# Performance work log

Measured on AMD Instinct MI355X. Metric: run time of the kernel, lower is better.

## Reference

```python
import jax, jax.numpy as jnp
import numpy as np

C_IN = 12      # total channels (rgb-noised + hidden)
C_NOISE = 3    # noise-prediction channels
HID = 128      # rule-MLP hidden size
PERC = 48      # perception channels (depthwise, 48/12 = 4 filters per channel)
TDIM = 256     # sinusoidal time-embedding dim


def setup_inputs() -> dict:
    key = jax.random.key(0)
    ks = jax.random.split(key, 12)
    B, H, W = 16, 256, 256
    x = jax.random.normal(ks[0], (B, C_NOISE, H, W), jnp.float32)
    hidden_channels = jax.random.normal(ks[1], (B, C_IN - C_NOISE, H, W), jnp.float32)
    t = jax.random.randint(ks[2], (B,), 0, 1000)
    # depthwise 3x3 perceive conv: torch weight shape [out=48, in/groups=1, 3, 3]
    w_perceive = jax.random.normal(ks[3], (PERC, 1, 3, 3), jnp.float32) * 0.1
    b_perceive = jax.random.normal(ks[4], (PERC,), jnp.float32) * 0.01
    # 1x1 convs of the rule network, stored as [out, in]
    w1 = jax.random.normal(ks[5], (HID, PERC), jnp.float32) * 0.1
    b1 = jax.random.normal(ks[6], (HID,), jnp.float32) * 0.01
    w2 = jax.random.normal(ks[7], (HID, HID), jnp.float32) * 0.05
    b2 = jax.random.normal(ks[8], (HID,), jnp.float32) * 0.01
    # conv3 is zero-initialized in the original; random here for test coverage
    w3 = jax.random.normal(ks[9], (C_IN, HID), jnp.float32) * 0.05
    # time embedding Linear(256 -> c_noise)
    w_time = jax.random.normal(ks[10], (C_NOISE, TDIM), jnp.float32) * 0.1
    b_time = jax.random.normal(ks[11], (C_NOISE,), jnp.float32) * 0.01
    return dict(x=x, hidden_channels=hidden_channels, t=t,
                w_perceive=w_perceive, b_perceive=b_perceive,
                w1=w1, b1=b1, w2=w2, b2=b2, w3=w3,
                w_time=w_time, b_time=b_time)


def _pos_encoding(t, channels):
    # t: [B] int -> [B, channels] sinusoidal embedding (torch repeat-then-scale layout)
    inv_freq = 1.0 / (10000.0 ** (jnp.arange(0, channels, 2, dtype=jnp.float32) / channels))
    ang = t.astype(jnp.float32)[:, None] * inv_freq  # [B, channels//2]
    return jnp.concatenate([jnp.sin(ang), jnp.cos(ang)], axis=-1)


def reference(x, hidden_channels, t, w_perceive, b_perceive, w1, b1, w2, b2, w3, w_time, b_time):
    # concat noised channels with hidden state channels -> [B, 12, H, W]
    xf = jnp.concatenate([x, hidden_channels], axis=1)
    # depthwise 3x3 conv, 'same' padding, groups = C_IN
    perc = jax.lax.conv_general_dilated(
        xf, w_perceive, window_strides=(1, 1), padding='SAME',
        feature_group_count=C_IN,
        dimension_numbers=('NCHW', 'OIHW', 'NCHW')) + b_perceive[None, :, None, None]
    # rule network: three 1x1 convs (pointwise MLP) with ReLUs
    h = jax.nn.relu(jnp.einsum('bchw,oc->bohw', perc, w1) + b1[None, :, None, None])
    h = jax.nn.relu(jnp.einsum('bchw,oc->bohw', h, w2) + b2[None, :, None, None])
    out = jnp.einsum('bchw,oc->bohw', h, w3)  # no bias
    # time embedding: sinusoidal -> SiLU -> Linear -> broadcast over H, W
    pe = _pos_encoding(t, TDIM)                       # [B, 256]
    emb = jax.nn.silu(pe) @ w_time.T + b_time         # [B, 3]
    noise_prediction = out[:, :C_NOISE] + emb[:, :, None, None]
    hidden_out = out[:, C_NOISE:]
    return (hidden_out, noise_prediction)
```

## Files before the change

### kernel.cpp

```cpp
#include <hip/hip_runtime.h>


#define ACT_S 136
#define NOISE_BASE 9437184

#define WSF_OFF 17408
#define WSF_B1 0
#define WSF_B2 128
#define WSF_EMB 256

typedef short bf16x8 __attribute__((ext_vector_type(8)));
typedef float f32x4 __attribute__((ext_vector_type(4)));

__device__ __forceinline__ short f2bf(float f) {
    union { float f; unsigned u; } cv; cv.f = f;
    unsigned r = cv.u + 0x7FFFu + ((cv.u >> 16) & 1u);
    return (short)(r >> 16);
}
__device__ __forceinline__ unsigned pk2bf(float f0, float f1) {
    union { float f; unsigned u; } a, b; a.f = f0; b.f = f1;
    return __builtin_amdgcn_perm(b.u + 0x8000u, a.u + 0x8000u, 0x07060302u);
}

__device__ __forceinline__ int permch(int f) {
    return (f & ~31) + 8 * ((f & 15) >> 2) + 4 * ((f >> 4) & 1) + (f & 3);
}

__global__ void prep_emb_kernel(const float* __restrict__ wpg, const float* __restrict__ bpg,
                                const float* __restrict__ w1g, const float* __restrict__ b1g,
                                const float* __restrict__ w2g, const float* __restrict__ b2g,
                                const float* __restrict__ w3g,
                                const int* __restrict__ t,
                                const float* __restrict__ wt, const float* __restrict__ bt,
                                short* __restrict__ wsb, float* __restrict__ wsf)
{
    const int bid = blockIdx.x, tid = threadIdx.x;
    if (bid < 64) {
        int i = bid * 256 + tid;
        int f = i >> 7, kk = i & 127;
        int o = permch(f);
        int qq = kk >> 5, r = kk & 31;
        float v = 0.f;
        if (r < 30 && (r % 10) < 9) {
            int c3 = r / 10, k = r % 10;
            int ic = 3 * qq + c3;
            #pragma unroll
            for (int j = 0; j < 4; ++j)
                v += w1g[o * 48 + 4 * ic + j] * wpg[(4 * ic + j) * 9 + k];
        }
        wsb[i] = f2bf(v);
        return;
    }
    if (bid < 128) {
        int i = (bid - 64) * 256 + tid;
        int f = i >> 7, col = i & 127;
        wsb[16384 + i] = f2bf(w2g[permch(f) * 128 + col]);
        return;
    }
    if (bid == 128) {
        for (int j = tid; j < 2048; j += 256)
            wsb[32768 + j] = (j < 1536) ? f2bf(w3g[j]) : (short)0;
        return;
    }
    if (bid == 129) {
        if (tid < 128) {
            float s = b1g[tid];
            #pragma unroll 4
            for (int c = 0; c < 48; ++c) s += w1g[tid * 48 + c] * bpg[c];
            wsf[WSF_B1 + tid] = s;
        } else {
            wsf[WSF_B2 + (tid - 128)] = b2g[tid - 128];
        }
        return;
    }
    int b = bid - 130;
    int lane = threadIdx.x;
    if (lane >= 64) return;
    float tv = (float)t[b];
    float s0 = 0.f, s1 = 0.f, s2 = 0.f;
    const float LOG1E4 = 9.210340371976184f;
    #pragma unroll
    for (int ii = 0; ii < 2; ++ii) {
        int i = lane + ii * 64;
        float invf = __expf(-LOG1E4 * (float)i * (1.0f / 128.0f));
        float ang = tv * invf;
        float sn = sinf(ang), cs = cosf(ang);
        float ss = sn / (1.0f + __expf(-sn));
        float sc = cs / (1.0f + __expf(-cs));
        s0 += ss * wt[0 * 256 + i] + sc * wt[0 * 256 + i + 128];
        s1 += ss * wt[1 * 256 + i] + sc * wt[1 * 256 + i + 128];
        s2 += ss * wt[2 * 256 + i] + sc * wt[2 * 256 + i + 128];
    }
    #pragma unroll
    for (int off = 32; off; off >>= 1) {
        s0 += __shfl_down(s0, off);
        s1 += __shfl_down(s1, off);
        s2 += __shfl_down(s2, off);
    }
    if (lane == 0) {
        wsf[WSF_EMB + b * 3 + 0] = s0 + bt[0];
        wsf[WSF_EMB + b * 3 + 1] = s1 + bt[1];
        wsf[WSF_EMB + b * 3 + 2] = s2 + bt[2];
    }
}

__global__ __launch_bounds__(256, 3) void canet_main(
    const float* __restrict__ xg,
    const float* __restrict__ hg,
    const short* __restrict__ wsb,
    const float* __restrict__ wsf,
    float* __restrict__ outg)
{
    __shared__ __align__(16) short bufA[64 * ACT_S];
    __shared__ __align__(16) short h1S[64 * ACT_S];
    __shared__ __align__(16) short w3_s[16 * 128];
    __shared__ __align__(16) float bias_s[256];

    const int tid = threadIdx.x;
    const int b = blockIdx.x >> 8;
    const int y = blockIdx.x & 255;

    bias_s[tid] = wsf[WSF_B1 + tid];
    for (int i = tid; i < 2048; i += 256) {
        int row = i >> 7, col = i & 127;
        w3_s[(row << 7) + (col ^ ((row & 7) << 3))] = wsb[32768 + i];
    }

    const int wv = tid >> 6;
    const int lane = tid & 63;
    const int m = lane & 15;
    const int q = lane >> 4;

    bf16x8 w1f[2][4], w2f[2][4];
    #pragma unroll
    for (int j = 0; j < 2; ++j) {
        int n = wv * 32 + j * 16 + m;
        #pragma unroll
        for (int ks = 0; ks < 4; ++ks) {
            w1f[j][ks] = *(const bf16x8*)(wsb + n * 128 + ks * 32 + q * 8);
            w2f[j][ks] = *(const bf16x8*)(wsb + 16384 + n * 128 + ks * 32 + q * 8);
        }
    }
    const float embv = (m < 3) ? wsf[WSF_EMB + b * 3 + m] : 0.0f;

    const float* src3[3];
    #pragma unroll
    for (int i3 = 0; i3 < 3; ++i3) {
        int ic = 3 * q + i3;
        src3[i3] = (ic < 3) ? (xg + (((size_t)b * 3 + ic) << 16))
                            : (hg + (((size_t)b * 9 + (ic - 3)) << 16));
    }
    int yoff[3]; bool yokk[3];
    #pragma unroll
    for (int ky = 0; ky < 3; ++ky) {
        int yy = y + ky - 1;
        yokk[ky] = (yy >= 0) && (yy < 256);
        yoff[ky] = (yokk[ky] ? yy : y) * 256;
    }

    auto load_taps = [&](float (&tp)[27], int pxl) {
        const int xm1 = pxl - (pxl > 0);
        const int xp1 = pxl + (pxl < 255);
        #pragma unroll
        for (int i3 = 0; i3 < 3; ++i3) {
            #pragma unroll
            for (int ky = 0; ky < 3; ++ky) {
                const float* rp = src3[i3] + yoff[ky];
                tp[i3 * 9 + ky * 3 + 0] = rp[xm1];
                tp[i3 * 9 + ky * 3 + 1] = rp[pxl];
                tp[i3 * 9 + ky * 3 + 2] = rp[xp1];
            }
        }
    };

    const int w3sw = (m & 7) << 3;

    float tp[27];
    load_taps(tp, wv * 16 + m);

    __syncthreads();

    for (int it = 0; it < 4; ++it) {
        const int x0 = it * 64;
        const int px = x0 + wv * 16 + m;

        {
            const bool okl = (px > 0), okr = (px < 255);
            short* prow = bufA + (wv * 16 + m) * ACT_S + 32 * q;
            unsigned rr[16];
            rr[15] = 0u;
            #pragma unroll
            for (int i3 = 0; i3 < 3; ++i3) {
                float tm[9];
                #pragma unroll
                for (int ky = 0; ky < 3; ++ky) {
                    int o = i3 * 9 + ky * 3;
                    tm[ky * 3 + 0] = (yokk[ky] && okl) ? tp[o + 0] : 0.0f;
                    tm[ky * 3 + 1] = yokk[ky] ? tp[o + 1] : 0.0f;
                    tm[ky * 3 + 2] = (yokk[ky] && okr) ? tp[o + 2] : 0.0f;
                }
                rr[5 * i3 + 0] = pk2bf(tm[0], tm[1]);
                rr[5 * i3 + 1] = pk2bf(tm[2], tm[3]);
                rr[5 * i3 + 2] = pk2bf(tm[4], tm[5]);
                rr[5 * i3 + 3] = pk2bf(tm[6], tm[7]);
                rr[5 * i3 + 4] = pk2bf(tm[8], 0.0f);
            }
            #pragma unroll
            for (int w = 0; w < 4; ++w) {
                uint4 v; v.x = rr[4*w]; v.y = rr[4*w+1]; v.z = rr[4*w+2]; v.w = rr[4*w+3];
                *(uint4*)(prow + 8 * w) = v;
            }
        }
        __syncthreads();

        if (it < 3) load_taps(tp, px + 64);

        #pragma unroll
        for (int nt = 0; nt < 4; ++nt) {
            f32x4 c0 = *(const f32x4*)(bias_s + wv * 32 + 8 * q);
            f32x4 c1 = *(const f32x4*)(bias_s + wv * 32 + 8 * q + 4);
            #pragma unroll
            for (int ks = 0; ks < 4; ++ks) {
                bf16x8 p = *(const bf16x8*)(bufA + (nt * 16 + m) * ACT_S + ks * 32 + q * 8);
                c0 = __builtin_amdgcn_mfma_f32_16x16x32_bf16(w1f[0][ks], p, c0, 0, 0, 0);
                c1 = __builtin_amdgcn_mfma_f32_16x16x32_bf16(w1f[1][ks], p, c1, 0, 0, 0);
            }
            short* drow = h1S + (nt * 16 + m) * ACT_S + wv * 32 + 8 * q;
            uint4 pk4;
            pk4.x = pk2bf(fmaxf(c0[0], 0.f), fmaxf(c0[1], 0.f));
            pk4.y = pk2bf(fmaxf(c0[2], 0.f), fmaxf(c0[3], 0.f));
            pk4.z = pk2bf(fmaxf(c1[0], 0.f), fmaxf(c1[1], 0.f));
            pk4.w = pk2bf(fmaxf(c1[2], 0.f), fmaxf(c1[3], 0.f));
            *(uint4*)drow = pk4;
        }
        __syncthreads();

        #pragma unroll
        for (int nt = 0; nt < 4; ++nt) {
            f32x4 c0 = *(const f32x4*)(bias_s + 128 + wv * 32 + 8 * q);
            f32x4 c1 = *(const f32x4*)(bias_s + 128 + wv * 32 + 8 * q + 4);
            #pragma unroll
            for (int ks = 0; ks < 4; ++ks) {
                bf16x8 a = *(const bf16x8*)(h1S + (nt * 16 + m) * ACT_S + ks * 32 + q * 8);
                c0 = __builtin_amdgcn_mfma_f32_16x16x32_bf16(w2f[0][ks], a, c0, 0, 0, 0);
                c1 = __builtin_amdgcn_mfma_f32_16x16x32_bf16(w2f[1][ks], a, c1, 0, 0, 0);
            }
            short* drow = bufA + (nt * 16 + m) * ACT_S + wv * 32 + 8 * q;
            uint4 pk4;
            pk4.x = pk2bf(fmaxf(c0[0], 0.f), fmaxf(c0[1], 0.f));
            pk4.y = pk2bf(fmaxf(c0[2], 0.f), fmaxf(c0[3], 0.f));
            pk4.z = pk2bf(fmaxf(c1[0], 0.f), fmaxf(c1[1], 0.f));
            pk4.w = pk2bf(fmaxf(c1[2], 0.f), fmaxf(c1[3], 0.f));
            *(uint4*)drow = pk4;
        }
        __syncthreads();

        {
            f32x4 acc = {0.f, 0.f, 0.f, 0.f};
            #pragma unroll
            for (int ks = 0; ks < 4; ++ks) {
                bf16x8 a = *(const bf16x8*)(bufA + (wv * 16 + m) * ACT_S + ks * 32 + q * 8);
                bf16x8 w3k = *(const bf16x8*)(w3_s + (m << 7) + ((ks * 32 + q * 8) ^ w3sw));
                acc = __builtin_amdgcn_mfma_f32_16x16x32_bf16(a, w3k, acc, 0, 0, 0);
            }
            if (m < 12) {
                int xx0 = x0 + wv * 16 + q * 4;
                size_t idx;
                if (m < 3) {
                    idx = (size_t)NOISE_BASE + (((size_t)b * 3 + m) << 16) + (size_t)y * 256 + xx0;
                } else {
                    idx = (((size_t)b * 9 + (m - 3)) << 16) + (size_t)y * 256 + xx0;
                }
                f32x4 vst = {acc[0] + embv, acc[1] + embv, acc[2] + embv, acc[3] + embv};
                *(f32x4*)(outg + idx) = vst;
            }
        }
        __syncthreads();
    }
}

extern "C" void kernel_launch(void* const* d_in, const int* in_sizes, int n_in,
                              void* d_out, int out_size, void* d_ws, size_t ws_size,
                              hipStream_t stream) {
    const float* xg  = (const float*)d_in[0];
    const float* hg  = (const float*)d_in[1];
    const int*   tg  = (const int*)  d_in[2];
    const float* wpg = (const float*)d_in[3];
    const float* bpg = (const float*)d_in[4];
    const float* w1g = (const float*)d_in[5];
    const float* b1g = (const float*)d_in[6];
    const float* w2g = (const float*)d_in[7];
    const float* b2g = (const float*)d_in[8];
    const float* w3g = (const float*)d_in[9];
    const float* wtg = (const float*)d_in[10];
    const float* btg = (const float*)d_in[11];
    float* outg = (float*)d_out;
    short* wsb  = (short*)d_ws;
    float* wsf  = (float*)d_ws + WSF_OFF;

    prep_emb_kernel<<<146, 256, 0, stream>>>(wpg, bpg, w1g, b1g, w2g, b2g, w3g,
                                             tg, wtg, btg, wsb, wsf);
    canet_main<<<4096, 256, 0, stream>>>(xg, hg, wsb, wsf, outg);
}
```

Baseline: 204.9 us.

## Retile MFMA layers to 64-channel by 32-pixel warp tiles for operand reuse

Changes the per-wave tiling of the two 128x128 MLP layers. Each wave previously computed 32 output channels across all 64 pixels; now it computes 64 channels across 32 pixels, which halves the LDS activation reads per MFMA. The host-side weight permutation is updated to match the new output packing. The cost is twice as many resident weight-fragment registers, so launch bounds drop from 3 to 2 blocks per SM, which lowers occupancy.

```diff
diff --git a/kernel.cpp b/kernel.cpp
--- a/kernel.cpp
+++ b/kernel.cpp
@@ -22,8 +22,8 @@
     return __builtin_amdgcn_perm(b.u + 0x8000u, a.u + 0x8000u, 0x07060302u);
 }
 
-__device__ __forceinline__ int permch(int f) {
-    return (f & ~31) + 8 * ((f & 15) >> 2) + 4 * ((f >> 4) & 1) + (f & 3);
+__device__ __forceinline__ int permch64(int f) {
+    return (f & ~63) + 16 * ((f >> 2) & 3) + 4 * ((f >> 4) & 3) + (f & 3);
 }
 
 __global__ void prep_emb_kernel(const float* __restrict__ wpg, const float* __restrict__ bpg,
@@ -38,7 +38,7 @@
     if (bid < 64) {
         int i = bid * 256 + tid;
         int f = i >> 7, kk = i & 127;
-        int o = permch(f);
+        int o = permch64(f);
         int qq = kk >> 5, r = kk & 31;
         float v = 0.f;
         if (r < 30 && (r % 10) < 9) {
@@ -54,7 +54,7 @@
     if (bid < 128) {
         int i = (bid - 64) * 256 + tid;
         int f = i >> 7, col = i & 127;
-        wsb[16384 + i] = f2bf(w2g[permch(f) * 128 + col]);
+        wsb[16384 + i] = f2bf(w2g[permch64(f) * 128 + col]);
         return;
     }
     if (bid == 128) {
@@ -104,7 +104,7 @@
     }
 }
 
-__global__ __launch_bounds__(256, 3) void canet_main(
+__global__ __launch_bounds__(256, 2) void canet_main(
     const float* __restrict__ xg,
     const float* __restrict__ hg,
     const short* __restrict__ wsb,
@@ -130,15 +130,17 @@
     const int lane = tid & 63;
     const int m = lane & 15;
     const int q = lane >> 4;
-
-    bf16x8 w1f[2][4], w2f[2][4];
-    #pragma unroll
-    for (int j = 0; j < 2; ++j) {
-        int n = wv * 32 + j * 16 + m;
+    const int wc = wv >> 1;
+    const int wp = wv & 1;
+
+    bf16x8 w1f[4][4], w2f[4][4];
+    #pragma unroll
+    for (int jt = 0; jt < 4; ++jt) {
+        int n = wc * 64 + jt * 16 + m;
         #pragma unroll
         for (int ks = 0; ks < 4; ++ks) {
-            w1f[j][ks] = *(const bf16x8*)(wsb + n * 128 + ks * 32 + q * 8);
-            w2f[j][ks] = *(const bf16x8*)(wsb + 16384 + n * 128 + ks * 32 + q * 8);
+            w1f[jt][ks] = *(const bf16x8*)(wsb + n * 128 + ks * 32 + q * 8);
+            w2f[jt][ks] = *(const bf16x8*)(wsb + 16384 + n * 128 + ks * 32 + q * 8);
         }
     }
     const float embv = (m < 3) ? wsf[WSF_EMB + b * 3 + m] : 0.0f;
@@ -216,42 +218,62 @@
         if (it < 3) load_taps(tp, px + 64);
 
         #pragma unroll
-        for (int nt = 0; nt < 4; ++nt) {
-            f32x4 c0 = *(const f32x4*)(bias_s + wv * 32 + 8 * q);
-            f32x4 c1 = *(const f32x4*)(bias_s + wv * 32 + 8 * q + 4);
+        for (int nt = 0; nt < 2; ++nt) {
+            const int prow = (wp * 32 + nt * 16 + m) * ACT_S;
+            f32x4 d0 = *(const f32x4*)(bias_s + wc * 64 + 16 * q + 0);
+            f32x4 d1 = *(const f32x4*)(bias_s + wc * 64 + 16 * q + 4);
+            f32x4 d2 = *(const f32x4*)(bias_s + wc * 64 + 16 * q + 8);
+            f32x4 d3 = *(const f32x4*)(bias_s + wc * 64 + 16 * q + 12);
             #pragma unroll
             for (int ks = 0; ks < 4; ++ks) {
-                bf16x8 p = *(const bf16x8*)(bufA + (nt * 16 + m) * ACT_S + ks * 32 + q * 8);
-                c0 = __builtin_amdgcn_mfma_f32_16x16x32_bf16(w1f[0][ks], p, c0, 0, 0, 0);
-                c1 = __builtin_amdgcn_mfma_f32_16x16x32_bf16(w1f[1][ks], p, c1, 0, 0, 0);
-            }
-            short* drow = h1S + (nt * 16 + m) * ACT_S + wv * 32 + 8 * q;
-            uint4 pk4;
-            pk4.x = pk2bf(fmaxf(c0[0], 0.f), fmaxf(c0[1], 0.f));
-            pk4.y = pk2bf(fmaxf(c0[2], 0.f), fmaxf(c0[3], 0.f));
-            pk4.z = pk2bf(fmaxf(c1[0], 0.f), fmaxf(c1[1], 0.f));
-            pk4.w = pk2bf(fmaxf(c1[2], 0.f), fmaxf(c1[3], 0.f));
-            *(uint4*)drow = pk4;
+                bf16x8 p = *(const bf16x8*)(bufA + prow + ks * 32 + q * 8);
+                d0 = __builtin_amdgcn_mfma_f32_16x16x32_bf16(w1f[0][ks], p, d0, 0, 0, 0);
+                d1 = __builtin_amdgcn_mfma_f32_16x16x32_bf16(w1f[1][ks], p, d1, 0, 0, 0);
+                d2 = __builtin_amdgcn_mfma_f32_16x16x32_bf16(w1f[2][ks], p, d2, 0, 0, 0);
+                d3 = __builtin_amdgcn_mfma_f32_16x16x32_bf16(w1f[3][ks], p, d3, 0, 0, 0);
+            }
+            short* drow = h1S + prow + wc * 64 + 16 * q;
+            uint4 A, B;
+            A.x = pk2bf(fmaxf(d0[0], 0.f), fmaxf(d0[1], 0.f));
+            A.y = pk2bf(fmaxf(d0[2], 0.f), fmaxf(d0[3], 0.f));
+            A.z = pk2bf(fmaxf(d1[0], 0.f), fmaxf(d1[1], 0.f));
+            A.w = pk2bf(fmaxf(d1[2], 0.f), fmaxf(d1[3], 0.f));
+            B.x = pk2bf(fmaxf(d2[0], 0.f), fmaxf(d2[1], 0.f));
+            B.y = pk2bf(fmaxf(d2[2], 0.f), fmaxf(d2[3], 0.f));
+            B.z = pk2bf(fmaxf(d3[0], 0.f), fmaxf(d3[1], 0.f));
+            B.w = pk2bf(fmaxf(d3[2], 0.f), fmaxf(d3[3], 0.f));
+            *(uint4*)drow = A;
+            *(uint4*)(drow + 8) = B;
         }
         __syncthreads();
 
         #pragma unroll
-        for (int nt = 0; nt < 4; ++nt) {
-            f32x4 c0 = *(const f32x4*)(bias_s + 128 + wv * 32 + 8 * q);
-            f32x4 c1 = *(const f32x4*)(bias_s + 128 + wv * 32 + 8 * q + 4);
+        for (int nt = 0; nt < 2; ++nt) {
+            const int prow = (wp * 32 + nt * 16 + m) * ACT_S;
+            f32x4 d0 = *(const f32x4*)(bias_s + 128 + wc * 64 + 16 * q + 0);
+            f32x4 d1 = *(const f32x4*)(bias_s + 128 + wc * 64 + 16 * q + 4);
+            f32x4 d2 = *(const f32x4*)(bias_s + 128 + wc * 64 + 16 * q + 8);
+            f32x4 d3 = *(const f32x4*)(bias_s + 128 + wc * 64 + 16 * q + 12);
             #pragma unroll
             for (int ks = 0; ks < 4; ++ks) {
-                bf16x8 a = *(const bf16x8*)(h1S + (nt * 16 + m) * ACT_S + ks * 32 + q * 8);
-                c0 = __builtin_amdgcn_mfma_f32_16x16x32_bf16(w2f[0][ks], a, c0, 0, 0, 0);
-                c1 = __builtin_amdgcn_mfma_f32_16x16x32_bf16(w2f[1][ks], a, c1, 0, 0, 0);
-            }
-            short* drow = bufA + (nt * 16 + m) * ACT_S + wv * 32 + 8 * q;
-            uint4 pk4;
-            pk4.x = pk2bf(fmaxf(c0[0], 0.f), fmaxf(c0[1], 0.f));
-            pk4.y = pk2bf(fmaxf(c0[2], 0.f), fmaxf(c0[3], 0.f));
-            pk4.z = pk2bf(fmaxf(c1[0], 0.f), fmaxf(c1[1], 0.f));
-            pk4.w = pk2bf(fmaxf(c1[2], 0.f), fmaxf(c1[3], 0.f));
-            *(uint4*)drow = pk4;
+                bf16x8 a = *(const bf16x8*)(h1S + prow + ks * 32 + q * 8);
+                d0 = __builtin_amdgcn_mfma_f32_16x16x32_bf16(w2f[0][ks], a, d0, 0, 0, 0);
+                d1 = __builtin_amdgcn_mfma_f32_16x16x32_bf16(w2f[1][ks], a, d1, 0, 0, 0);
+                d2 = __builtin_amdgcn_mfma_f32_16x16x32_bf16(w2f[2][ks], a, d2, 0, 0, 0);
+                d3 = __builtin_amdgcn_mfma_f32_16x16x32_bf16(w2f[3][ks], a, d3, 0, 0, 0);
+            }
+            short* drow = bufA + prow + wc * 64 + 16 * q;
+            uint4 A, B;
+            A.x = pk2bf(fmaxf(d0[0], 0.f), fmaxf(d0[1], 0.f));
+            A.y = pk2bf(fmaxf(d0[2], 0.f), fmaxf(d0[3], 0.f));
+            A.z = pk2bf(fmaxf(d1[0], 0.f), fmaxf(d1[1], 0.f));
+            A.w = pk2bf(fmaxf(d1[2], 0.f), fmaxf(d1[3], 0.f));
+            B.x = pk2bf(fmaxf(d2[0], 0.f), fmaxf(d2[1], 0.f));
+            B.y = pk2bf(fmaxf(d2[2], 0.f), fmaxf(d2[3], 0.f));
+            B.z = pk2bf(fmaxf(d3[0], 0.f), fmaxf(d3[1], 0.f));
+            B.w = pk2bf(fmaxf(d3[2], 0.f), fmaxf(d3[3], 0.f));
+            *(uint4*)drow = A;
+            *(uint4*)(drow + 8) = B;
         }
         __syncthreads();
 
```

New measurement: 246.1 us. 20.1% more time.
